# Performance work log

Hardware: AMD Instinct MI355X
Metric: run time of the kernel (lower is better)

Reference implementation:

```python
import jax, jax.numpy as jnp
import numpy as np

N = 50000      # nodes
E = 1600000    # edges (avg degree 32)
DIN, DH, DOUT = 256, 128, 64


def gcn_conv(x, W, b, row, col, w, n):
    """One GCNConv layer (self-loops already appended to row/col/w).
    row = source nodes, col = target nodes; aggregate at targets."""
    xw = x @ W                                        # [n, d_out]
    deg = jax.ops.segment_sum(w, col, num_segments=n)  # in-degree weighted
    dinv = jnp.where(deg > 0, jax.lax.rsqrt(deg), 0.0)
    norm = dinv[row] * w * dinv[col]                  # [E+n]
    msg = norm[:, None] * xw[row]                     # [E+n, d_out] gather
    out = jax.ops.segment_sum(msg, col, num_segments=n)
    return out + b


def setup_inputs() -> dict:
    key = jax.random.key(0)
    k = jax.random.split(key, 6)
    x = jax.random.normal(k[0], (N, DIN), dtype=jnp.float32)
    edge_index = jax.random.randint(k[1], (2, E), 0, N)
    edge_weight = jax.random.uniform(k[2], (E,), dtype=jnp.float32)
    W1 = jax.random.normal(k[3], (DIN, DH), dtype=jnp.float32) * (1.0 / np.sqrt(DIN))
    b1 = jnp.zeros((DH,), dtype=jnp.float32)
    W2 = jax.random.normal(k[4], (DH, DOUT), dtype=jnp.float32) * (1.0 / np.sqrt(DH))
    b2 = jnp.zeros((DOUT,), dtype=jnp.float32)
    return {"x": x, "edge_index": edge_index, "edge_weight": edge_weight,
            "W1": W1, "b1": b1, "W2": W2, "b2": b2}


def reference(x, edge_index, edge_weight, W1, b1, W2, b2):
    n = x.shape[0]
    loops = jnp.arange(n, dtype=edge_index.dtype)
    row = jnp.concatenate([edge_index[0], loops])
    col = jnp.concatenate([edge_index[1], loops])
    w = jnp.concatenate([edge_weight, jnp.ones((n,), dtype=edge_weight.dtype)])
    h = gcn_conv(x, W1, b1, row, col, w, n)
    h = jax.nn.relu(h)
    # dropout(p=0.2) is identity in eval mode
    h = gcn_conv(h, W2, b2, row, col, w, n)
    return jax.nn.log_softmax(h, axis=-1)
```

## Files before the change

### kernel.cpp

```cpp
#include <hip/hip_runtime.h>
#include <hip/hip_bf16.h>
#include <cstddef>


#define DIN 256
#define DH  128
#define DOUT 64
#define NPB 100
#define NBMAX 512

typedef __bf16 bf16x8 __attribute__((ext_vector_type(8)));
typedef float f32x4 __attribute__((ext_vector_type(4)));

__device__ __forceinline__ float bflo(unsigned u) { return __uint_as_float(u << 16); }
__device__ __forceinline__ float bfhi(unsigned u) { return __uint_as_float(u & 0xffff0000u); }
__device__ __forceinline__ unsigned short f2bf(float f) {
    unsigned u = __float_as_uint(f);
    unsigned r = (u + 0x7fffu + ((u >> 16) & 1u)) >> 16;
    return (unsigned short)r;
}

__global__ void prep_w_kernel(const float* __restrict__ W1, const float* __restrict__ W2,
                              unsigned short* __restrict__ wt1, unsigned short* __restrict__ wt2) {
    int i = blockIdx.x * 256 + threadIdx.x;
    if (i < DH * DIN) {
        int nn = i >> 8, k = i & 255;
        wt1[i] = f2bf(W1[k * DH + nn]);
    } else {
        int j = i - DH * DIN;
        if (j < DOUT * DH) {
            int nn = j >> 7, k = j & 127;
            wt2[j] = f2bf(W2[k * DOUT + nn]);
        }
    }
}

__launch_bounds__(256)
__global__ void hist_kernel(const int* __restrict__ col, int* __restrict__ bh,
                            int E, int Ec, int NB) {
    __shared__ int hist[NBMAX];
    int p = blockIdx.x, t = threadIdx.x;
    for (int b = t; b < NB; b += 256) hist[b] = 0;
    __syncthreads();
    int s = p * Ec, e = min(s + Ec, E);
    for (int i = s + t; i < e; i += 256) atomicAdd(&hist[col[i] / NPB], 1);
    __syncthreads();
    for (int b = t; b < NB; b += 256) bh[p * NB + b] = hist[b];
}

__launch_bounds__(512)
__global__ void colscan_kernel(int* __restrict__ bh, int* __restrict__ btotal,
                               int P, int NB) {
    __shared__ int arr[512];
    int b = blockIdx.x, t = threadIdx.x;
    arr[t] = (t < P) ? bh[t * NB + b] : 0;
    __syncthreads();
    for (int off = 1; off < 512; off <<= 1) {
        int v = (t >= off) ? arr[t - off] : 0;
        __syncthreads();
        arr[t] += v;
        __syncthreads();
    }
    int excl = (t == 0) ? 0 : arr[t - 1];
    if (t < P) bh[t * NB + b] = excl;
    if (t == P - 1) btotal[b] = arr[t];
}

__launch_bounds__(512)
__global__ void basescan_kernel(const int* __restrict__ btotal, int* __restrict__ bbase,
                                int* __restrict__ rowptr, int NB, int n, int E) {
    __shared__ int arr[512];
    int t = threadIdx.x;
    arr[t] = (t < NB) ? btotal[t] : 0;
    __syncthreads();
    for (int off = 1; off < 512; off <<= 1) {
        int v = (t >= off) ? arr[t - off] : 0;
        __syncthreads();
        arr[t] += v;
        __syncthreads();
    }
    int excl = (t == 0) ? 0 : arr[t - 1];
    if (t <= NB) bbase[t] = excl;
    if (t == 511) rowptr[n] = E;
}

__launch_bounds__(256)
__global__ void scatter_kernel(const int* __restrict__ row, const int* __restrict__ col,
                               const float* __restrict__ w, const int* __restrict__ bh,
                               const int* __restrict__ bbase, int2* __restrict__ part,
                               int E, int Ec, int NB) {
    __shared__ int cur[NBMAX];
    int p = blockIdx.x, t = threadIdx.x;
    for (int b = t; b < NB; b += 256) cur[b] = bbase[b] + bh[p * NB + b];
    __syncthreads();
    int s = p * Ec, e = min(s + Ec, E);
    for (int i = s + t; i < e; i += 256) {
        int c = col[i];
        int r = row[i];
        int b = c / NPB;
        int pos = atomicAdd(&cur[b], 1);
        part[pos] = make_int2(r | ((c - b * NPB) << 16), __float_as_int(w[i]));
    }
}

__launch_bounds__(256)
__global__ void bucket_csr_kernel(const int2* __restrict__ part, const int* __restrict__ bbase,
                                  float* __restrict__ dinv, int* __restrict__ rowptr,
                                  int2* __restrict__ final_e, int n) {
    __shared__ int   hist[NPB];
    __shared__ float wsum[NPB];
    __shared__ int   nbase[NPB];
    __shared__ int   cur[NPB];
    int b = blockIdx.x, t = threadIdx.x;
    if (t < NPB) { hist[t] = 0; wsum[t] = 0.0f; }
    __syncthreads();
    int s = bbase[b], e = bbase[b + 1];
    for (int i = s + t; i < e; i += 256) {
        int2 rec = part[i];
        int cl = rec.x >> 16;
        atomicAdd(&hist[cl], 1);
        atomicAdd(&wsum[cl], __int_as_float(rec.y));
    }
    __syncthreads();
    if (t == 0) {
        int run = 0;
        for (int k = 0; k < NPB; ++k) { nbase[k] = run; run += hist[k]; }
    }
    __syncthreads();
    if (t < NPB) {
        int node = b * NPB + t;
        if (node < n) {
            dinv[node] = rsqrtf(1.0f + wsum[t]);
            rowptr[node] = s + nbase[t];
        }
        cur[t] = nbase[t];
    }
    __syncthreads();
    for (int i = s + t; i < e; i += 256) {
        int2 rec = part[i];
        int cl = rec.x >> 16;
        int q = s + atomicAdd(&cur[cl], 1);
        final_e[q] = make_int2(rec.x & 0xffff, rec.y);
    }
}

template <int K, int M>
__launch_bounds__(256)
__global__ void gemm_mfma_kernel(const float* __restrict__ A,
                                 const unsigned short* __restrict__ Wt,
                                 const float* __restrict__ scale,
                                 unsigned short* __restrict__ C, int N) {
    constexpr int BK = 64, LD = BK + 8;
    constexpr int WN = M / 4;
    constexpr int NT = WN / 16;
    constexpr int CLD = M + 8;
    constexpr int SM = (64 * LD + M * LD) > (64 * CLD) ? (64 * LD + M * LD) : (64 * CLD);
    __shared__ unsigned short smem[SM];
    __shared__ float sdv[64];
    unsigned short* As = smem;
    unsigned short* Bs = smem + 64 * LD;

    const int tid = threadIdx.x;
    const int row0 = blockIdx.x * 64;
    const int lane = tid & 63;
    const int quad = lane >> 4, r16 = lane & 15;
    const int n0 = (tid >> 6) * WN;

    if (tid < 64) {
        int r = row0 + tid;
        sdv[tid] = (r < N) ? scale[r] : 0.0f;
    }

    f32x4 acc[4][NT];
#pragma unroll
    for (int mt = 0; mt < 4; ++mt)
#pragma unroll
        for (int nt = 0; nt < NT; ++nt)
            acc[mt][nt] = (f32x4){0.f, 0.f, 0.f, 0.f};

    for (int k0 = 0; k0 < K; k0 += BK) {
#pragma unroll
        for (int j = 0; j < 4; ++j) {
            int idx = tid + j * 256;
            int m = idx >> 4;
            int q = idx & 15;
            int gr = row0 + m;
            float4 v = make_float4(0.f, 0.f, 0.f, 0.f);
            if (gr < N) v = *(const float4*)&A[(size_t)gr * K + k0 + q * 4];
            ushort4 s4;
            s4.x = f2bf(v.x); s4.y = f2bf(v.y); s4.z = f2bf(v.z); s4.w = f2bf(v.w);
            *(ushort4*)&As[m * LD + q * 4] = s4;
        }
#pragma unroll
        for (int j = 0; j < M * 8 / 256; ++j) {
            int idx = tid + j * 256;
            int nn = idx >> 3;
            int q = idx & 7;
            uint4 v = *(const uint4*)&Wt[(size_t)nn * K + k0 + q * 8];
            *(uint4*)&Bs[nn * LD + q * 8] = v;
        }
        __syncthreads();
#pragma unroll
        for (int ks = 0; ks < BK / 32; ++ks) {
            bf16x8 af[4], bfr[NT];
#pragma unroll
            for (int nt = 0; nt < NT; ++nt)
                bfr[nt] = *(const bf16x8*)&Bs[(n0 + nt * 16 + r16) * LD + ks * 32 + quad * 8];
#pragma unroll
            for (int mt = 0; mt < 4; ++mt)
                af[mt] = *(const bf16x8*)&As[(mt * 16 + r16) * LD + ks * 32 + quad * 8];
#pragma unroll
            for (int mt = 0; mt < 4; ++mt)
#pragma unroll
                for (int nt = 0; nt < NT; ++nt)
                    acc[mt][nt] = __builtin_amdgcn_mfma_f32_16x16x32_bf16(
                        af[mt], bfr[nt], acc[mt][nt], 0, 0, 0);
        }
        __syncthreads();
    }
    unsigned short* Cs = smem;
#pragma unroll
    for (int mt = 0; mt < 4; ++mt) {
#pragma unroll
        for (int i = 0; i < 4; ++i) {
            int r = mt * 16 + quad * 4 + i;
            float sc = sdv[r];
#pragma unroll
            for (int nt = 0; nt < NT; ++nt)
                Cs[r * CLD + n0 + nt * 16 + r16] = f2bf(acc[mt][nt][i] * sc);
        }
    }
    __syncthreads();
#pragma unroll
    for (int j = 0; j < 64 * M / 8 / 256; ++j) {
        int idx = tid + j * 256;
        int r = idx / (M / 8);
        int q = idx % (M / 8);
        int gr = row0 + r;
        if (gr < N) {
            uint4 v = *(const uint4*)&Cs[r * CLD + q * 8];
            *(uint4*)&C[(size_t)gr * M + q * 8] = v;
        }
    }
}

__launch_bounds__(256)
__global__ void agg1_kernel(const uint2* __restrict__ xw,
                            const int* __restrict__ rowptr,
                            const int2* __restrict__ edge,
                            const float* __restrict__ dinv,
                            const float* __restrict__ bias,
                            float* __restrict__ out, int n) {
    int node = blockIdx.x * 4 + (threadIdx.x >> 6);
    if (node >= n) return;
    int lane = threadIdx.x & 63;
    int half = lane >> 5, sub = lane & 31;
    float a0 = 0.f, a1 = 0.f, a2 = 0.f, a3 = 0.f;
    if (half == 0) {
        uint2 u = xw[(size_t)node * 32 + sub];
        a0 = bflo(u.x); a1 = bfhi(u.x); a2 = bflo(u.y); a3 = bfhi(u.y);
    }
    int p = rowptr[node], p1 = rowptr[node + 1];
    for (; p + 8 <= p1; p += 8) {
        int2 e0 = edge[p + half],     e1 = edge[p + 2 + half];
        int2 e2 = edge[p + 4 + half], e3 = edge[p + 6 + half];
        uint2 v0 = xw[(size_t)e0.x * 32 + sub];
        uint2 v1 = xw[(size_t)e1.x * 32 + sub];
        uint2 v2 = xw[(size_t)e2.x * 32 + sub];
        uint2 v3 = xw[(size_t)e3.x * 32 + sub];
        float w0 = __int_as_float(e0.y), w1 = __int_as_float(e1.y);
        float w2 = __int_as_float(e2.y), w3 = __int_as_float(e3.y);
        a0 += w0 * bflo(v0.x) + w1 * bflo(v1.x) + w2 * bflo(v2.x) + w3 * bflo(v3.x);
        a1 += w0 * bfhi(v0.x) + w1 * bfhi(v1.x) + w2 * bfhi(v2.x) + w3 * bfhi(v3.x);
        a2 += w0 * bflo(v0.y) + w1 * bflo(v1.y) + w2 * bflo(v2.y) + w3 * bflo(v3.y);
        a3 += w0 * bfhi(v0.y) + w1 * bfhi(v1.y) + w2 * bfhi(v2.y) + w3 * bfhi(v3.y);
    }
    for (; p + 2 <= p1; p += 2) {
        int2 e0 = edge[p + half];
        uint2 v0 = xw[(size_t)e0.x * 32 + sub];
        float w0 = __int_as_float(e0.y);
        a0 += w0 * bflo(v0.x); a1 += w0 * bfhi(v0.x);
        a2 += w0 * bflo(v0.y); a3 += w0 * bfhi(v0.y);
    }
    if (p < p1 && half == 0) {
        int2 e0 = edge[p];
        uint2 v0 = xw[(size_t)e0.x * 32 + sub];
        float w0 = __int_as_float(e0.y);
        a0 += w0 * bflo(v0.x); a1 += w0 * bfhi(v0.x);
        a2 += w0 * bflo(v0.y); a3 += w0 * bfhi(v0.y);
    }
    a0 += __shfl_xor(a0, 32); a1 += __shfl_xor(a1, 32);
    a2 += __shfl_xor(a2, 32); a3 += __shfl_xor(a3, 32);
    float di = dinv[node];
    float4 b = ((const float4*)bias)[sub];
    a0 = fmaxf(di * a0 + b.x, 0.f);
    a1 = fmaxf(di * a1 + b.y, 0.f);
    a2 = fmaxf(di * a2 + b.z, 0.f);
    a3 = fmaxf(di * a3 + b.w, 0.f);
    if (half == 0)
        ((float4*)out)[(size_t)node * 32 + sub] = make_float4(a0, a1, a2, a3);
}

__launch_bounds__(256)
__global__ void agg2_kernel(const uint2* __restrict__ xw,
                            const int* __restrict__ rowptr,
                            const int2* __restrict__ edge,
                            const float* __restrict__ dinv,
                            const float* __restrict__ bias,
                            float* __restrict__ out, int n) {
    int node = blockIdx.x * 4 + (threadIdx.x >> 6);
    if (node >= n) return;
    int lane = threadIdx.x & 63;
    int qw = lane >> 4, sub = lane & 15;
    float a0 = 0.f, a1 = 0.f, a2 = 0.f, a3 = 0.f;
    if (qw == 0) {
        uint2 u = xw[(size_t)node * 16 + sub];
        a0 = bflo(u.x); a1 = bfhi(u.x); a2 = bflo(u.y); a3 = bfhi(u.y);
    }
    int p = rowptr[node], p1 = rowptr[node + 1];
    for (; p + 8 <= p1; p += 8) {
        int2 e0 = edge[p + qw], e1 = edge[p + 4 + qw];
        uint2 v0 = xw[(size_t)e0.x * 16 + sub];
        uint2 v1 = xw[(size_t)e1.x * 16 + sub];
        float w0 = __int_as_float(e0.y), w1 = __int_as_float(e1.y);
        a0 += w0 * bflo(v0.x) + w1 * bflo(v1.x);
        a1 += w0 * bfhi(v0.x) + w1 * bfhi(v1.x);
        a2 += w0 * bflo(v0.y) + w1 * bflo(v1.y);
        a3 += w0 * bfhi(v0.y) + w1 * bfhi(v1.y);
    }
    for (; p + 4 <= p1; p += 4) {
        int2 e0 = edge[p + qw];
        uint2 v0 = xw[(size_t)e0.x * 16 + sub];
        float w0 = __int_as_float(e0.y);
        a0 += w0 * bflo(v0.x); a1 += w0 * bfhi(v0.x);
        a2 += w0 * bflo(v0.y); a3 += w0 * bfhi(v0.y);
    }
    int rem = p1 - p;
    if (qw < rem) {
        int2 e0 = edge[p + qw];
        uint2 v0 = xw[(size_t)e0.x * 16 + sub];
        float w0 = __int_as_float(e0.y);
        a0 += w0 * bflo(v0.x); a1 += w0 * bfhi(v0.x);
        a2 += w0 * bflo(v0.y); a3 += w0 * bfhi(v0.y);
    }
    a0 += __shfl_xor(a0, 32); a1 += __shfl_xor(a1, 32);
    a2 += __shfl_xor(a2, 32); a3 += __shfl_xor(a3, 32);
    a0 += __shfl_xor(a0, 16); a1 += __shfl_xor(a1, 16);
    a2 += __shfl_xor(a2, 16); a3 += __shfl_xor(a3, 16);
    float di = dinv[node];
    float4 b = ((const float4*)bias)[sub];
    a0 = di * a0 + b.x; a1 = di * a1 + b.y;
    a2 = di * a2 + b.z; a3 = di * a3 + b.w;
    float m = fmaxf(fmaxf(a0, a1), fmaxf(a2, a3));
#pragma unroll
    for (int off = 8; off > 0; off >>= 1) m = fmaxf(m, __shfl_xor(m, off));
    float s = __expf(a0 - m) + __expf(a1 - m) + __expf(a2 - m) + __expf(a3 - m);
#pragma unroll
    for (int off = 8; off > 0; off >>= 1) s += __shfl_xor(s, off);
    float lse = m + __logf(s);
    if (qw == 0)
        ((float4*)out)[(size_t)node * 16 + sub] =
            make_float4(a0 - lse, a1 - lse, a2 - lse, a3 - lse);
}

extern "C" void kernel_launch(void* const* d_in, const int* in_sizes, int n_in,
                              void* d_out, int out_size, void* d_ws, size_t ws_size,
                              hipStream_t stream) {
    const float* x  = (const float*)d_in[0];
    const int*   ei = (const int*)d_in[1];
    const float* ew = (const float*)d_in[2];
    const float* W1 = (const float*)d_in[3];
    const float* b1 = (const float*)d_in[4];
    const float* W2 = (const float*)d_in[5];
    const float* b2 = (const float*)d_in[6];
    float* out = (float*)d_out;

    const int n = in_sizes[0] / DIN;
    const int E = in_sizes[2];
    const int* row = ei;
    const int* col = ei + E;

    const int NB = (n + NPB - 1) / NPB;
    const int P  = NB;
    const int Ec = (E + P - 1) / P;

    char* ptr = (char*)d_ws;
    auto alloc = [&](size_t bytes) -> void* {
        void* r = (void*)ptr;
        ptr += (bytes + 255) & ~(size_t)255;
        return r;
    };
    int*   bh     = (int*)  alloc((size_t)P * NB * 4);
    int*   btotal = (int*)  alloc((size_t)NB * 4);
    int*   bbase  = (int*)  alloc((size_t)(NB + 1) * 4);
    int*   rowptr = (int*)  alloc((size_t)(n + 1) * 4);
    float* dinv   = (float*)alloc((size_t)n * 4);
    int2*  edge   = (int2*) alloc((size_t)E * 8);
    unsigned short* xw1 = (unsigned short*)alloc((size_t)n * DH * 2);
    unsigned short* wt1 = (unsigned short*)alloc((size_t)DH * DIN * 2);
    unsigned short* wt2 = (unsigned short*)alloc((size_t)DOUT * DH * 2);
    char* tail = (char*)alloc((size_t)n * DH * 4);
    int2*  part = (int2*)tail;
    float* h1   = (float*)tail;
    unsigned short* xw2 = xw1;

    const int nb_g = (n + 63) / 64;
    const int nb_a = (n + 3) / 4;

    prep_w_kernel<<<(DH * DIN + DOUT * DH + 255) / 256, 256, 0, stream>>>(W1, W2, wt1, wt2);
    hist_kernel<<<P, 256, 0, stream>>>(col, bh, E, Ec, NB);
    colscan_kernel<<<NB, 512, 0, stream>>>(bh, btotal, P, NB);
    basescan_kernel<<<1, 512, 0, stream>>>(btotal, bbase, rowptr, NB, n, E);
    scatter_kernel<<<P, 256, 0, stream>>>(row, col, ew, bh, bbase, part, E, Ec, NB);
    bucket_csr_kernel<<<NB, 256, 0, stream>>>(part, bbase, dinv, rowptr, edge, n);

    gemm_mfma_kernel<DIN, DH><<<nb_g, 256, 0, stream>>>(x, wt1, dinv, xw1, n);
    agg1_kernel<<<nb_a, 256, 0, stream>>>((const uint2*)xw1, rowptr, edge, dinv, b1, h1, n);
    gemm_mfma_kernel<DH, DOUT><<<nb_g, 256, 0, stream>>>(h1, wt2, dinv, xw2, n);
    agg2_kernel<<<nb_a, 256, 0, stream>>>((const uint2*)xw2, rowptr, edge, dinv, b2, out, n);
}
```

Before: 286.6 us.

## Fuse layer-1 aggregation with layer-2 GEMM and merge weight prep into histogram

The layer-1 aggregation kernel now handles 16 nodes per block. It keeps the ReLU output as bf16 in shared memory and runs the 128x64 layer-2 MFMA GEMM in place, writing the scaled xw2 directly. This removes the fp32 h1 round trip through global memory and one kernel launch. Weight transposition is folded into extra blocks of the histogram kernel, and the serial per-bucket prefix sum in bucket_csr becomes a parallel shared-memory scan. In exchange, each wave handles 4 nodes sequentially, which may reduce latency hiding in the gather, and h1 is rounded to bf16 before the GEMM.

Result: no change. 291.6 us (+1.8%).

```diff
diff --git a/kernel.cpp b/kernel.cpp
--- a/kernel.cpp
+++ b/kernel.cpp
@@ -20,26 +20,27 @@
     return (unsigned short)r;
 }
 
-__global__ void prep_w_kernel(const float* __restrict__ W1, const float* __restrict__ W2,
-                              unsigned short* __restrict__ wt1, unsigned short* __restrict__ wt2) {
-    int i = blockIdx.x * 256 + threadIdx.x;
-    if (i < DH * DIN) {
-        int nn = i >> 8, k = i & 255;
-        wt1[i] = f2bf(W1[k * DH + nn]);
-    } else {
-        int j = i - DH * DIN;
-        if (j < DOUT * DH) {
-            int nn = j >> 7, k = j & 127;
-            wt2[j] = f2bf(W2[k * DOUT + nn]);
-        }
-    }
-}
-
-__launch_bounds__(256)
-__global__ void hist_kernel(const int* __restrict__ col, int* __restrict__ bh,
-                            int E, int Ec, int NB) {
+__launch_bounds__(256)
+__global__ void hist_prep_kernel(const int* __restrict__ col, int* __restrict__ bh,
+                                 int E, int Ec, int NB, int P,
+                                 const float* __restrict__ W1, const float* __restrict__ W2,
+                                 unsigned short* __restrict__ wt1, unsigned short* __restrict__ wt2) {
     __shared__ int hist[NBMAX];
     int p = blockIdx.x, t = threadIdx.x;
+    if (p >= P) {
+        int i = (p - P) * 256 + t;
+        if (i < DH * DIN) {
+            int nn = i >> 8, k = i & 255;
+            wt1[i] = f2bf(W1[k * DH + nn]);
+        } else {
+            int j = i - DH * DIN;
+            if (j < DOUT * DH) {
+                int nn = j >> 7, k = j & 127;
+                wt2[j] = f2bf(W2[k * DOUT + nn]);
+            }
+        }
+        return;
+    }
     for (int b = t; b < NB; b += 256) hist[b] = 0;
     __syncthreads();
     int s = p * Ec, e = min(s + Ec, E);
@@ -109,7 +110,7 @@
                                   int2* __restrict__ final_e, int n) {
     __shared__ int   hist[NPB];
     __shared__ float wsum[NPB];
-    __shared__ int   nbase[NPB];
+    __shared__ int   arr[256];
     __shared__ int   cur[NPB];
     int b = blockIdx.x, t = threadIdx.x;
     if (t < NPB) { hist[t] = 0; wsum[t] = 0.0f; }
@@ -122,18 +123,23 @@
         atomicAdd(&wsum[cl], __int_as_float(rec.y));
     }
     __syncthreads();
-    if (t == 0) {
-        int run = 0;
-        for (int k = 0; k < NPB; ++k) { nbase[k] = run; run += hist[k]; }
-    }
-    __syncthreads();
+    int hv = (t < NPB) ? hist[t] : 0;
+    arr[t] = hv;
+    __syncthreads();
+    for (int off = 1; off < 256; off <<= 1) {
+        int v = (t >= off) ? arr[t - off] : 0;
+        __syncthreads();
+        arr[t] += v;
+        __syncthreads();
+    }
     if (t < NPB) {
+        int nb = arr[t] - hv;
+        cur[t] = nb;
         int node = b * NPB + t;
         if (node < n) {
             dinv[node] = rsqrtf(1.0f + wsum[t]);
-            rowptr[node] = s + nbase[t];
-        }
-        cur[t] = nbase[t];
+            rowptr[node] = s + nb;
+        }
     }
     __syncthreads();
     for (int i = s + t; i < e; i += 256) {
@@ -245,60 +251,107 @@
 }
 
 __launch_bounds__(256)
-__global__ void agg1_kernel(const uint2* __restrict__ xw,
-                            const int* __restrict__ rowptr,
-                            const int2* __restrict__ edge,
-                            const float* __restrict__ dinv,
-                            const float* __restrict__ bias,
-                            float* __restrict__ out, int n) {
-    int node = blockIdx.x * 4 + (threadIdx.x >> 6);
-    if (node >= n) return;
-    int lane = threadIdx.x & 63;
-    int half = lane >> 5, sub = lane & 31;
-    float a0 = 0.f, a1 = 0.f, a2 = 0.f, a3 = 0.f;
-    if (half == 0) {
-        uint2 u = xw[(size_t)node * 32 + sub];
-        a0 = bflo(u.x); a1 = bfhi(u.x); a2 = bflo(u.y); a3 = bfhi(u.y);
-    }
-    int p = rowptr[node], p1 = rowptr[node + 1];
-    for (; p + 8 <= p1; p += 8) {
-        int2 e0 = edge[p + half],     e1 = edge[p + 2 + half];
-        int2 e2 = edge[p + 4 + half], e3 = edge[p + 6 + half];
-        uint2 v0 = xw[(size_t)e0.x * 32 + sub];
-        uint2 v1 = xw[(size_t)e1.x * 32 + sub];
-        uint2 v2 = xw[(size_t)e2.x * 32 + sub];
-        uint2 v3 = xw[(size_t)e3.x * 32 + sub];
-        float w0 = __int_as_float(e0.y), w1 = __int_as_float(e1.y);
-        float w2 = __int_as_float(e2.y), w3 = __int_as_float(e3.y);
-        a0 += w0 * bflo(v0.x) + w1 * bflo(v1.x) + w2 * bflo(v2.x) + w3 * bflo(v3.x);
-        a1 += w0 * bfhi(v0.x) + w1 * bfhi(v1.x) + w2 * bfhi(v2.x) + w3 * bfhi(v3.x);
-        a2 += w0 * bflo(v0.y) + w1 * bflo(v1.y) + w2 * bflo(v2.y) + w3 * bflo(v3.y);
-        a3 += w0 * bfhi(v0.y) + w1 * bfhi(v1.y) + w2 * bfhi(v2.y) + w3 * bfhi(v3.y);
-    }
-    for (; p + 2 <= p1; p += 2) {
-        int2 e0 = edge[p + half];
-        uint2 v0 = xw[(size_t)e0.x * 32 + sub];
-        float w0 = __int_as_float(e0.y);
-        a0 += w0 * bflo(v0.x); a1 += w0 * bfhi(v0.x);
-        a2 += w0 * bflo(v0.y); a3 += w0 * bfhi(v0.y);
-    }
-    if (p < p1 && half == 0) {
-        int2 e0 = edge[p];
-        uint2 v0 = xw[(size_t)e0.x * 32 + sub];
-        float w0 = __int_as_float(e0.y);
-        a0 += w0 * bflo(v0.x); a1 += w0 * bfhi(v0.x);
-        a2 += w0 * bflo(v0.y); a3 += w0 * bfhi(v0.y);
-    }
-    a0 += __shfl_xor(a0, 32); a1 += __shfl_xor(a1, 32);
-    a2 += __shfl_xor(a2, 32); a3 += __shfl_xor(a3, 32);
-    float di = dinv[node];
-    float4 b = ((const float4*)bias)[sub];
-    a0 = fmaxf(di * a0 + b.x, 0.f);
-    a1 = fmaxf(di * a1 + b.y, 0.f);
-    a2 = fmaxf(di * a2 + b.z, 0.f);
-    a3 = fmaxf(di * a3 + b.w, 0.f);
-    if (half == 0)
-        ((float4*)out)[(size_t)node * 32 + sub] = make_float4(a0, a1, a2, a3);
+__global__ void agg1_fused_kernel(const uint2* __restrict__ xw,
+                                  const int* __restrict__ rowptr,
+                                  const int2* __restrict__ edge,
+                                  const float* __restrict__ dinv,
+                                  const float* __restrict__ bias,
+                                  const unsigned short* __restrict__ wt2,
+                                  unsigned short* __restrict__ xw2,
+                                  int n) {
+    __shared__ unsigned short h1s[16][136];
+    __shared__ unsigned short c2s[16][72];
+    __shared__ float sdv[16];
+    const int w = threadIdx.x >> 6;
+    const int lane = threadIdx.x & 63;
+    const int half = lane >> 5, sub = lane & 31;
+    const int node0 = blockIdx.x * 16;
+#pragma unroll 1
+    for (int r = 0; r < 4; ++r) {
+        const int lrow = w * 4 + r;
+        int node = node0 + lrow;
+        if (node < n) {
+            float a0 = 0.f, a1 = 0.f, a2 = 0.f, a3 = 0.f;
+            if (half == 0) {
+                uint2 u = xw[(size_t)node * 32 + sub];
+                a0 = bflo(u.x); a1 = bfhi(u.x); a2 = bflo(u.y); a3 = bfhi(u.y);
+            }
+            int p = rowptr[node], p1 = rowptr[node + 1];
+            for (; p + 8 <= p1; p += 8) {
+                int2 e0 = edge[p + half],     e1 = edge[p + 2 + half];
+                int2 e2 = edge[p + 4 + half], e3 = edge[p + 6 + half];
+                uint2 v0 = xw[(size_t)e0.x * 32 + sub];
+                uint2 v1 = xw[(size_t)e1.x * 32 + sub];
+                uint2 v2 = xw[(size_t)e2.x * 32 + sub];
+                uint2 v3 = xw[(size_t)e3.x * 32 + sub];
+                float w0 = __int_as_float(e0.y), w1 = __int_as_float(e1.y);
+                float w2 = __int_as_float(e2.y), w3 = __int_as_float(e3.y);
+                a0 += w0 * bflo(v0.x) + w1 * bflo(v1.x) + w2 * bflo(v2.x) + w3 * bflo(v3.x);
+                a1 += w0 * bfhi(v0.x) + w1 * bfhi(v1.x) + w2 * bfhi(v2.x) + w3 * bfhi(v3.x);
+                a2 += w0 * bflo(v0.y) + w1 * bflo(v1.y) + w2 * bflo(v2.y) + w3 * bflo(v3.y);
+                a3 += w0 * bfhi(v0.y) + w1 * bfhi(v1.y) + w2 * bfhi(v2.y) + w3 * bfhi(v3.y);
+            }
+            for (; p + 2 <= p1; p += 2) {
+                int2 e0 = edge[p + half];
+                uint2 v0 = xw[(size_t)e0.x * 32 + sub];
+                float w0 = __int_as_float(e0.y);
+                a0 += w0 * bflo(v0.x); a1 += w0 * bfhi(v0.x);
+                a2 += w0 * bflo(v0.y); a3 += w0 * bfhi(v0.y);
+            }
+            if (p < p1 && half == 0) {
+                int2 e0 = edge[p];
+                uint2 v0 = xw[(size_t)e0.x * 32 + sub];
+                float w0 = __int_as_float(e0.y);
+                a0 += w0 * bflo(v0.x); a1 += w0 * bfhi(v0.x);
+                a2 += w0 * bflo(v0.y); a3 += w0 * bfhi(v0.y);
+            }
+            a0 += __shfl_xor(a0, 32); a1 += __shfl_xor(a1, 32);
+            a2 += __shfl_xor(a2, 32); a3 += __shfl_xor(a3, 32);
+            float di = dinv[node];
+            float4 b = ((const float4*)bias)[sub];
+            a0 = fmaxf(di * a0 + b.x, 0.f);
+            a1 = fmaxf(di * a1 + b.y, 0.f);
+            a2 = fmaxf(di * a2 + b.z, 0.f);
+            a3 = fmaxf(di * a3 + b.w, 0.f);
+            if (half == 0) {
+                ushort4 s4;
+                s4.x = f2bf(a0); s4.y = f2bf(a1); s4.z = f2bf(a2); s4.w = f2bf(a3);
+                *(ushort4*)&h1s[lrow][sub * 4] = s4;
+            }
+            if (lane == 0) sdv[lrow] = di;
+        } else {
+            if (half == 0) {
+                ushort4 z; z.x = z.y = z.z = z.w = 0;
+                *(ushort4*)&h1s[lrow][sub * 4] = z;
+            }
+            if (lane == 0) sdv[lrow] = 0.f;
+        }
+    }
+    __syncthreads();
+    const int quad = lane >> 4, r16 = lane & 15;
+    const int n0 = w * 16;
+    f32x4 acc = (f32x4){0.f, 0.f, 0.f, 0.f};
+#pragma unroll
+    for (int ks = 0; ks < 4; ++ks) {
+        bf16x8 af = *(const bf16x8*)&h1s[r16][ks * 32 + quad * 8];
+        bf16x8 bf = *(const bf16x8*)&wt2[(size_t)(n0 + r16) * 128 + ks * 32 + quad * 8];
+        acc = __builtin_amdgcn_mfma_f32_16x16x32_bf16(af, bf, acc, 0, 0, 0);
+    }
+#pragma unroll
+    for (int i = 0; i < 4; ++i) {
+        int rowi = quad * 4 + i;
+        c2s[rowi][n0 + r16] = f2bf(acc[i] * sdv[rowi]);
+    }
+    __syncthreads();
+    int idx = threadIdx.x;
+    if (idx < 128) {
+        int row = idx >> 3, q = idx & 7;
+        int node = node0 + row;
+        if (node < n) {
+            uint4 v = *(const uint4*)&c2s[row][q * 8];
+            *(uint4*)&xw2[(size_t)node * 64 + q * 8] = v;
+        }
+    }
 }
 
 __launch_bounds__(256)
@@ -397,25 +450,24 @@
     float* dinv   = (float*)alloc((size_t)n * 4);
     int2*  edge   = (int2*) alloc((size_t)E * 8);
     unsigned short* xw1 = (unsigned short*)alloc((size_t)n * DH * 2);
+    unsigned short* xw2 = (unsigned short*)alloc((size_t)n * DOUT * 2);
     unsigned short* wt1 = (unsigned short*)alloc((size_t)DH * DIN * 2);
     unsigned short* wt2 = (unsigned short*)alloc((size_t)DOUT * DH * 2);
-    char* tail = (char*)alloc((size_t)n * DH * 4);
-    int2*  part = (int2*)tail;
-    float* h1   = (float*)tail;
-    unsigned short* xw2 = xw1;
+    int2*  part   = (int2*) alloc((size_t)E * 8);
 
     const int nb_g = (n + 63) / 64;
     const int nb_a = (n + 3) / 4;
-
-    prep_w_kernel<<<(DH * DIN + DOUT * DH + 255) / 256, 256, 0, stream>>>(W1, W2, wt1, wt2);
-    hist_kernel<<<P, 256, 0, stream>>>(col, bh, E, Ec, NB);
+    const int nb_f = (n + 15) / 16;
+    const int PREPB = (DH * DIN + DOUT * DH + 255) / 256;
+
+    hist_prep_kernel<<<P + PREPB, 256, 0, stream>>>(col, bh, E, Ec, NB, P, W1, W2, wt1, wt2);
     colscan_kernel<<<NB, 512, 0, stream>>>(bh, btotal, P, NB);
     basescan_kernel<<<1, 512, 0, stream>>>(btotal, bbase, rowptr, NB, n, E);
     scatter_kernel<<<P, 256, 0, stream>>>(row, col, ew, bh, bbase, part, E, Ec, NB);
     bucket_csr_kernel<<<NB, 256, 0, stream>>>(part, bbase, dinv, rowptr, edge, n);
 
     gemm_mfma_kernel<DIN, DH><<<nb_g, 256, 0, stream>>>(x, wt1, dinv, xw1, n);
-    agg1_kernel<<<nb_a, 256, 0, stream>>>((const uint2*)xw1, rowptr, edge, dinv, b1, h1, n);
-    gemm_mfma_kernel<DH, DOUT><<<nb_g, 256, 0, stream>>>(h1, wt2, dinv, xw2, n);
+    agg1_fused_kernel<<<nb_f, 256, 0, stream>>>((const uint2*)xw1, rowptr, edge, dinv,
+                                                b1, wt2, xw2, n);
     agg2_kernel<<<nb_a, 256, 0, stream>>>((const uint2*)xw2, rowptr, edge, dinv, b2, out, n);
 }
```
